# Kernel optimization log

Measured on AMD Instinct MI355X. Metric: run time of the kernel, lower is better.

The kernel has to match this reference:

```python
import jax, jax.numpy as jnp
import numpy as np

HIDDEN = 2048
HEADS = 16
HEAD_DIM = HIDDEN // HEADS


def setup_inputs() -> dict:
    key = jax.random.key(0)
    ks = jax.random.split(key, 5)
    scale = 1.0 / np.sqrt(HIDDEN)
    x = jax.random.normal(ks[0], (2, 2048, HIDDEN), dtype=jnp.float32)
    wq = jax.random.normal(ks[1], (HIDDEN, HIDDEN), dtype=jnp.float32) * scale
    wk = jax.random.normal(ks[2], (HIDDEN, HIDDEN), dtype=jnp.float32) * scale
    wv = jax.random.normal(ks[3], (HIDDEN, HIDDEN), dtype=jnp.float32) * scale
    wo = jax.random.normal(ks[4], (HIDDEN, HIDDEN), dtype=jnp.float32) * scale
    return {"x": x, "wq": wq, "wk": wk, "wv": wv, "wo": wo}


def reference(x, wq, wk, wv, wo):
    B, S, D = x.shape
    # nn.Linear(w, bias=False): y = x @ w.T
    q = (x @ wq.T).reshape(B, S, HEADS, HEAD_DIM)
    k = (x @ wk.T).reshape(B, S, HEADS, HEAD_DIM)
    v = (x @ wv.T).reshape(B, S, HEADS, HEAD_DIM)
    scores = jnp.einsum("bqhd,bkhd->bhqk", q, k) / jnp.sqrt(
        jnp.asarray(HEAD_DIM, dtype=x.dtype)
    )
    causal_mask = jnp.triu(jnp.ones((S, S), dtype=bool), k=1)
    scores = jnp.where(causal_mask, -jnp.inf, scores)
    attn = jax.nn.softmax(scores, axis=-1)
    out = jnp.einsum("bhqk,bkhd->bqhd", attn, v).reshape(B, S, D)
    return out @ wo.T
```

## Files before the change

kernel.cpp:

```cpp
#include <hip/hip_runtime.h>
#include <hip/hip_bf16.h>
#include <math.h>

typedef unsigned short u16;
typedef __attribute__((ext_vector_type(8))) short bf16x8;
typedef __attribute__((ext_vector_type(4))) float f32x4;

__device__ static inline u16 f2bf(float f) {
  unsigned u = __float_as_uint(f);
  u += 0x7fff + ((u >> 16) & 1);
  return (u16)(u >> 16);
}

__device__ static inline void gload_lds16(const void* g, void* l) {
  __builtin_amdgcn_global_load_lds(
      (const __attribute__((address_space(1))) unsigned int*)g,
      (__attribute__((address_space(3))) unsigned int*)l, 16, 0, 0);
}

__device__ static inline void store_out(u16* p, float v)   { *p = f2bf(v); }
__device__ static inline void store_out(float* p, float v) { *p = v; }

__global__ void cvt_f32_bf16(const float* __restrict__ src, u16* __restrict__ dst, int n) {
  int stride = gridDim.x * blockDim.x;
  for (int i = blockIdx.x * blockDim.x + threadIdx.x; i * 8 < n; i += stride) {
    const float4* s4 = (const float4*)(src + (size_t)i * 8);
    float4 a = s4[0], b = s4[1];
    u16 t[8] = { f2bf(a.x), f2bf(a.y), f2bf(a.z), f2bf(a.w),
                 f2bf(b.x), f2bf(b.y), f2bf(b.z), f2bf(b.w) };
    *(bf16x8*)(dst + (size_t)i * 8) = *(bf16x8*)t;
  }
}

__global__ __launch_bounds__(512, 2)
void gemm_bt_256(const u16* __restrict__ A, const u16* __restrict__ Bm,
                 u16* __restrict__ C, int M, int N, int K) {
  __shared__ u16 Abuf[2][256 * 64];
  __shared__ u16 Bbuf[2][256 * 64];
  const int tid = threadIdx.x, lane = tid & 63, w = tid >> 6;
  const int wm = w >> 2, wn = w & 3;
  const int g = lane >> 4, l16 = lane & 15;

  const int per = gridDim.x >> 3;
  const int swz = ((int)blockIdx.x & 7) * per + ((int)blockIdx.x >> 3);
  const int nx = N >> 8;
  const int bx = swz % nx, by = swz / nx;
  const int brow = by << 8, bcol = bx << 8;
  const int nt = K >> 6;

  auto stage_half = [&](int sel, int kt, int d) {
    const u16* src = (sel < 2) ? A : Bm;
    const int rbase = (sel < 2) ? brow : bcol;
    const int h = sel & 1;
    char* lds = (char*)((sel < 2) ? Abuf[d] : Bbuf[d]) + h * 16384;
#pragma unroll
    for (int i = 0; i < 2; ++i) {
      int idx = i * 512 + tid;
      int r = h * 128 + (idx >> 3);
      int c = ((idx & 7) * 16) ^ ((r & 7) << 4);
      gload_lds16((const char*)(src + (size_t)(rbase + r) * K + kt * 64) + c,
                  lds + idx * 16);
    }
  };

  f32x4 acc[8][4] = {};
  bf16x8 afr[4][2], bfr0[2][2], bfr1[2][2];

  auto lda = [&](int d, int mf0) {
#pragma unroll
    for (int mf = 0; mf < 4; ++mf) {
      int r = wm * 128 + (mf0 + mf) * 16 + l16;
      const char* base = (const char*)Abuf[d] + r * 128;
      int sw = (r & 7) << 4;
#pragma unroll
      for (int ks = 0; ks < 2; ++ks)
        afr[mf][ks] = *(const bf16x8*)(base + ((ks * 64 + g * 16) ^ sw));
    }
  };
  auto ldb = [&](int d, int nf0, bf16x8 bf[2][2]) {
#pragma unroll
    for (int nf = 0; nf < 2; ++nf) {
      int r = wn * 64 + (nf0 + nf) * 16 + l16;
      const char* base = (const char*)Bbuf[d] + r * 128;
      int sw = (r & 7) << 4;
#pragma unroll
      for (int ks = 0; ks < 2; ++ks)
        bf[nf][ks] = *(const bf16x8*)(base + ((ks * 64 + g * 16) ^ sw));
    }
  };

#define WAIT_LGKM() do { \
    asm volatile("s_waitcnt lgkmcnt(0)" ::: "memory"); \
    __builtin_amdgcn_sched_barrier(0); } while (0)
#define QUAD(MF0, NF0, BFR) do { \
    __builtin_amdgcn_s_setprio(1); \
    _Pragma("unroll") for (int mf = 0; mf < 4; ++mf) \
    _Pragma("unroll") for (int nf = 0; nf < 2; ++nf) \
    _Pragma("unroll") for (int ks = 0; ks < 2; ++ks) \
      acc[MF0 + mf][NF0 + nf] = __builtin_amdgcn_mfma_f32_16x16x32_bf16( \
          afr[mf][ks], BFR[nf][ks], acc[MF0 + mf][NF0 + nf], 0, 0, 0); \
    __builtin_amdgcn_s_setprio(0); } while (0)

  stage_half(0, 0, 0); stage_half(1, 0, 0);
  stage_half(2, 0, 0); stage_half(3, 0, 0);
  stage_half(2, 1, 1); stage_half(3, 1, 1);
  asm volatile("s_waitcnt vmcnt(4)" ::: "memory");
  __builtin_amdgcn_sched_barrier(0);
  __builtin_amdgcn_s_barrier();

  for (int t = 0; t < nt; ++t) {
    const int cur = t & 1;
    lda(cur, 0); ldb(cur, 0, bfr0);
    if (t + 1 < nt) stage_half(0, t + 1, cur ^ 1);
    __builtin_amdgcn_s_barrier();
    WAIT_LGKM();
    QUAD(0, 0, bfr0);
    __builtin_amdgcn_s_barrier();
    ldb(cur, 2, bfr1);
    if (t + 1 < nt) stage_half(1, t + 1, cur ^ 1);
    __builtin_amdgcn_s_barrier();
    WAIT_LGKM();
    QUAD(0, 2, bfr1);
    __builtin_amdgcn_s_barrier();
    lda(cur, 4);
    if (t + 2 < nt) stage_half(2, t + 2, cur);
    __builtin_amdgcn_s_barrier();
    WAIT_LGKM();
    QUAD(4, 2, bfr1);
    __builtin_amdgcn_s_barrier();
    if (t + 2 < nt) stage_half(3, t + 2, cur);
    QUAD(4, 0, bfr0);
    if (t + 1 < nt) {
      if (t + 2 < nt) asm volatile("s_waitcnt vmcnt(4)" ::: "memory");
      else            asm volatile("s_waitcnt vmcnt(0)" ::: "memory");
      __builtin_amdgcn_sched_barrier(0);
      __builtin_amdgcn_s_barrier();
    }
  }
#undef WAIT_LGKM
#undef QUAD

  const size_t cb = (size_t)(brow + wm * 128) * N + bcol + wn * 64;
#pragma unroll
  for (int mf = 0; mf < 8; ++mf)
#pragma unroll
    for (int nf = 0; nf < 4; ++nf) {
      int col = nf * 16 + l16;
#pragma unroll
      for (int rr = 0; rr < 4; ++rr) {
        int row = mf * 16 + g * 4 + rr;
        C[cb + (size_t)row * N + col] = f2bf(acc[mf][nf][rr]);
      }
    }
}

template <typename OutT>
__global__ __launch_bounds__(256, 2)
void gemm_bt(const u16* __restrict__ A, const u16* __restrict__ Bm,
             OutT* __restrict__ C, int M, int N, int K) {
  __shared__ u16 As[128 * 32];
  __shared__ u16 Bs[128 * 32];
  const int tid = threadIdx.x;
  const int lane = tid & 63;
  const int w = tid >> 6, wr = w >> 1, wc = w & 1;
  const int g = lane >> 4, l16 = lane & 15;
  const int row0 = blockIdx.y * 128, col0 = blockIdx.x * 128;
  f32x4 acc[4][4] = {};

  for (int k0 = 0; k0 < K; k0 += 32) {
    __syncthreads();
#pragma unroll
    for (int i = 0; i < 2; ++i) {
      int idx = i * 256 + tid;
      int r = idx >> 2, c = (idx & 3) * 8;
      gload_lds16(A  + (size_t)(row0 + r) * K + k0 + c, As + idx * 8);
      gload_lds16(Bm + (size_t)(col0 + r) * K + k0 + c, Bs + idx * 8);
    }
    __syncthreads();
    bf16x8 af[4], bfr[4];
#pragma unroll
    for (int m2 = 0; m2 < 4; ++m2)
      af[m2] = *(const bf16x8*)(As + (wr * 64 + m2 * 16 + l16) * 32 + g * 8);
#pragma unroll
    for (int n2 = 0; n2 < 4; ++n2)
      bfr[n2] = *(const bf16x8*)(Bs + (wc * 64 + n2 * 16 + l16) * 32 + g * 8);
#pragma unroll
    for (int m2 = 0; m2 < 4; ++m2)
#pragma unroll
      for (int n2 = 0; n2 < 4; ++n2)
        acc[m2][n2] = __builtin_amdgcn_mfma_f32_16x16x32_bf16(af[m2], bfr[n2], acc[m2][n2], 0, 0, 0);
  }

#pragma unroll
  for (int m2 = 0; m2 < 4; ++m2)
#pragma unroll
    for (int n2 = 0; n2 < 4; ++n2) {
      int col = col0 + wc * 64 + n2 * 16 + l16;
#pragma unroll
      for (int r = 0; r < 4; ++r) {
        int row = row0 + wr * 64 + m2 * 16 + g * 4 + r;
        store_out(C + (size_t)row * N + col, acc[m2][n2][r]);
      }
    }
}

__global__ __launch_bounds__(256)
void transpose_v(const u16* __restrict__ QKV, u16* __restrict__ Vt) {
  __shared__ u16 t[64][72];
  const int tid = threadIdx.x;
  const int b = blockIdx.y >> 5;
  const int s0 = (blockIdx.y & 31) * 64;
  const int hd0 = blockIdx.x * 64;
  const int lr = tid >> 2, lc = (tid & 3) * 16;
  const u16* src = QKV + ((size_t)(b * 2048 + s0 + lr) * 6144 + 4096 + hd0 + lc);
  *(bf16x8*)&t[lr][lc]     = *(const bf16x8*)src;
  *(bf16x8*)&t[lr][lc + 8] = *(const bf16x8*)(src + 8);
  __syncthreads();
  u16 tmp[16];
#pragma unroll
  for (int j = 0; j < 16; ++j) tmp[j] = t[lc + j][lr];
  u16* dst = Vt + ((size_t)(b * 2048 + hd0 + lr) * 2048 + s0 + lc);
  *(bf16x8*)dst       = *(bf16x8*)tmp;
  *(bf16x8*)(dst + 8) = *(bf16x8*)(tmp + 8);
}

__global__ __launch_bounds__(256, 2)
void attn_fwd(const u16* __restrict__ QKV, const u16* __restrict__ Vt,
              u16* __restrict__ AO) {
  __shared__ u16 Ks[64 * 128];
  __shared__ u16 Vs[128 * 64];
  __shared__ u16 Ps[4][16 * 64];
  const int tid = threadIdx.x, lane = tid & 63, w = tid >> 6;
  const int g = lane >> 4, l16 = lane & 15;
  const int bh = blockIdx.y, b = bh >> 4, h = bh & 15;
  const int fold = blockIdx.x;

  for (int phase = 0; phase < 2; ++phase) {
    const int qt = phase == 0 ? fold : 31 - fold;
    const int q0 = qt * 64 + w * 16;

    bf16x8 qf[4];
    {
      const u16* qrow = QKV + ((size_t)(b * 2048 + q0 + l16) * 6144 + h * 128 + g * 8);
#pragma unroll
      for (int c = 0; c < 4; ++c) qf[c] = *(const bf16x8*)(qrow + c * 32);
    }
    f32x4 o[8] = {};
    float mrun[4] = {-INFINITY, -INFINITY, -INFINITY, -INFINITY};
    float lrun[4] = {0.f, 0.f, 0.f, 0.f};

    const int kv_last = qt * 64;
    for (int kv0 = 0; kv0 <= kv_last; kv0 += 64) {
      __syncthreads();
#pragma unroll
      for (int i = 0; i < 4; ++i) {
        int idx = i * 256 + tid;
        {
          int row = idx >> 4;
          int scolb = ((idx & 15) * 16) ^ ((row & 7) << 4);
          gload_lds16((const char*)QKV +
                          ((size_t)(b * 2048 + kv0 + row) * 6144 + 2048 + h * 128) * 2 + scolb,
                      (char*)Ks + idx * 16);
        }
        {
          int d = idx >> 3;
          int vcolb = ((idx & 7) * 16) ^ ((d & 7) << 4);
          gload_lds16((const char*)Vt + ((size_t)(bh * 128 + d) * 2048 + kv0) * 2 + vcolb,
                      (char*)Vs + idx * 16);
        }
      }
      __syncthreads();

      f32x4 s[4];
#pragma unroll
      for (int kb = 0; kb < 4; ++kb) {
        f32x4 a = {};
        int row = kb * 16 + l16;
        int swzk = (row & 7) << 4;
#pragma unroll
        for (int c = 0; c < 4; ++c) {
          bf16x8 kf = *(const bf16x8*)((const char*)Ks + row * 256 + ((c * 64 + g * 16) ^ swzk));
          a = __builtin_amdgcn_mfma_f32_16x16x32_bf16(qf[c], kf, a, 0, 0, 0);
        }
        s[kb] = a * 0.08838834764831845f;
      }
      if (kv0 == kv_last) {
#pragma unroll
        for (int kb = 0; kb < 4; ++kb)
#pragma unroll
          for (int r = 0; r < 4; ++r)
            if (kv0 + kb * 16 + l16 > q0 + g * 4 + r) s[kb][r] = -INFINITY;
      }

      float mnew[4], al[4], rs[4];
#pragma unroll
      for (int r = 0; r < 4; ++r) {
        float t = fmaxf(fmaxf(s[0][r], s[1][r]), fmaxf(s[2][r], s[3][r]));
        t = fmaxf(t, __shfl_xor(t, 1));
        t = fmaxf(t, __shfl_xor(t, 2));
        t = fmaxf(t, __shfl_xor(t, 4));
        t = fmaxf(t, __shfl_xor(t, 8));
        mnew[r] = fmaxf(mrun[r], t);
        al[r] = __expf(mrun[r] - mnew[r]);
        mrun[r] = mnew[r];
        rs[r] = 0.f;
      }
      {
        int prow = g * 4;
#pragma unroll
        for (int kb = 0; kb < 4; ++kb)
#pragma unroll
          for (int r = 0; r < 4; ++r) {
            float p = __expf(s[kb][r] - mnew[r]);
            rs[r] += p;
            int row = prow + r;
            int byteoff = (kb * 32 + l16 * 2) ^ ((row & 7) << 4);
            *(u16*)((char*)Ps[w] + row * 128 + byteoff) = f2bf(p);
          }
      }
#pragma unroll
      for (int r = 0; r < 4; ++r) {
        float t = rs[r];
        t += __shfl_xor(t, 1);
        t += __shfl_xor(t, 2);
        t += __shfl_xor(t, 4);
        t += __shfl_xor(t, 8);
        lrun[r] = lrun[r] * al[r] + t;
      }
#pragma unroll
      for (int db = 0; db < 8; ++db)
#pragma unroll
        for (int r = 0; r < 4; ++r) o[db][r] *= al[r];

      bf16x8 pa[2];
      {
        int swzp = (l16 & 7) << 4;
#pragma unroll
        for (int ks = 0; ks < 2; ++ks)
          pa[ks] = *(const bf16x8*)((const char*)Ps[w] + l16 * 128 + ((ks * 64 + g * 16) ^ swzp));
      }
#pragma unroll
      for (int db = 0; db < 8; ++db) {
        int row = db * 16 + l16;
        int swzv = (row & 7) << 4;
#pragma unroll
        for (int ks = 0; ks < 2; ++ks) {
          bf16x8 vf = *(const bf16x8*)((const char*)Vs + row * 128 + ((ks * 64 + g * 16) ^ swzv));
          o[db] = __builtin_amdgcn_mfma_f32_16x16x32_bf16(pa[ks], vf, o[db], 0, 0, 0);
        }
      }
    }

#pragma unroll
    for (int r = 0; r < 4; ++r) {
      float rl = 1.0f / lrun[r];
      int q = q0 + g * 4 + r;
#pragma unroll
      for (int db = 0; db < 8; ++db)
        AO[(size_t)(b * 2048 + q) * 2048 + h * 128 + db * 16 + l16] = f2bf(o[db][r] * rl);
    }
  }
}

extern "C" void kernel_launch(void* const* d_in, const int* in_sizes, int n_in,
                              void* d_out, int out_size, void* d_ws, size_t ws_size,
                              hipStream_t stream) {
  const float* x  = (const float*)d_in[0];
  const float* wq = (const float*)d_in[1];
  const float* wk = (const float*)d_in[2];
  const float* wv = (const float*)d_in[3];
  const float* wo = (const float*)d_in[4];
  float* out = (float*)d_out;

  char* ws = (char*)d_ws;
  u16* Xb   = (u16*)(ws);
  u16* Wqkv = (u16*)(ws + ((size_t)16 << 20));
  u16* Wob  = (u16*)(ws + ((size_t)40 << 20));
  u16* QKV  = (u16*)(ws + ((size_t)48 << 20));
  u16* Vt   = (u16*)(ws + ((size_t)96 << 20));
  u16* AO   = (u16*)(ws + ((size_t)112 << 20));

  auto cvt = [&](const float* s, u16* d, int n) {
    int blocks = (n / 8 + 255) / 256;
    if (blocks > 2048) blocks = 2048;
    cvt_f32_bf16<<<blocks, 256, 0, stream>>>(s, d, n);
  };
  cvt(x,  Xb,              2 * 2048 * 2048);
  cvt(wq, Wqkv,            2048 * 2048);
  cvt(wk, Wqkv + 4194304,  2048 * 2048);
  cvt(wv, Wqkv + 8388608,  2048 * 2048);
  cvt(wo, Wob,             2048 * 2048);

  gemm_bt_256<<<384, 512, 0, stream>>>(Xb, Wqkv, QKV, 4096, 6144, 2048);
  transpose_v<<<dim3(32, 64), 256, 0, stream>>>(QKV, Vt);
  attn_fwd<<<dim3(16, 32), 256, 0, stream>>>(QKV, Vt, AO);
  gemm_bt<float><<<dim3(16, 32), 256, 0, stream>>>(AO, Wob, out, 4096, 2048, 2048);
}
```

Before: 413.6 us.

## Generalize 256-row GEMM to templated N-tile; use it for QKV and output projection

Replaces the 256x256 QKV GEMM with a templated two-phase kernel whose N tile is 64*NF. QKV now uses 256x192 tiles (512 blocks instead of 384) for better CU fill. The simple 128x128 output-projection GEMM is replaced by the same pipelined kernel with 256x128 tiles. The pipeline is restructured into two halves per k-step with fewer barriers, and B is staged as a single block per step. Smaller N tiles reduce operand reuse per block.

```diff
diff --git a/kernel.cpp b/kernel.cpp
--- a/kernel.cpp
+++ b/kernel.cpp
@@ -32,39 +32,49 @@
   }
 }
 
+template <int NF, typename OutT>
 __global__ __launch_bounds__(512, 2)
-void gemm_bt_256(const u16* __restrict__ A, const u16* __restrict__ Bm,
-                 u16* __restrict__ C, int M, int N, int K) {
+void gemm2ph(const u16* __restrict__ A, const u16* __restrict__ Bm,
+             OutT* __restrict__ C, int M, int N, int K) {
+  constexpr int BN = NF * 64;
   __shared__ u16 Abuf[2][256 * 64];
-  __shared__ u16 Bbuf[2][256 * 64];
+  __shared__ u16 Bbuf[2][BN * 64];
   const int tid = threadIdx.x, lane = tid & 63, w = tid >> 6;
   const int wm = w >> 2, wn = w & 3;
   const int g = lane >> 4, l16 = lane & 15;
 
   const int per = gridDim.x >> 3;
   const int swz = ((int)blockIdx.x & 7) * per + ((int)blockIdx.x >> 3);
-  const int nx = N >> 8;
+  const int nx = N / BN;
   const int bx = swz % nx, by = swz / nx;
-  const int brow = by << 8, bcol = bx << 8;
+  const int brow = by << 8, bcol = bx * BN;
   const int nt = K >> 6;
 
-  auto stage_half = [&](int sel, int kt, int d) {
-    const u16* src = (sel < 2) ? A : Bm;
-    const int rbase = (sel < 2) ? brow : bcol;
-    const int h = sel & 1;
-    char* lds = (char*)((sel < 2) ? Abuf[d] : Bbuf[d]) + h * 16384;
+  auto stage_Ah = [&](int h, int kt, int d) {
+    char* lds = (char*)Abuf[d] + h * 16384;
 #pragma unroll
     for (int i = 0; i < 2; ++i) {
       int idx = i * 512 + tid;
       int r = h * 128 + (idx >> 3);
       int c = ((idx & 7) * 16) ^ ((r & 7) << 4);
-      gload_lds16((const char*)(src + (size_t)(rbase + r) * K + kt * 64) + c,
+      gload_lds16((const char*)(A + (size_t)(brow + r) * K + kt * 64) + c,
                   lds + idx * 16);
     }
   };
-
-  f32x4 acc[8][4] = {};
-  bf16x8 afr[4][2], bfr0[2][2], bfr1[2][2];
+  auto stage_B = [&](int kt, int d) {
+    char* lds = (char*)Bbuf[d];
+#pragma unroll
+    for (int i = 0; i < NF; ++i) {
+      int idx = i * 512 + tid;
+      int r = idx >> 3;
+      int c = ((idx & 7) * 16) ^ ((r & 7) << 4);
+      gload_lds16((const char*)(Bm + (size_t)(bcol + r) * K + kt * 64) + c,
+                  lds + idx * 16);
+    }
+  };
+
+  f32x4 acc[8][NF] = {};
+  bf16x8 afr[4][2], bfr[NF][2];
 
   auto lda = [&](int d, int mf0) {
 #pragma unroll
@@ -77,129 +87,80 @@
         afr[mf][ks] = *(const bf16x8*)(base + ((ks * 64 + g * 16) ^ sw));
     }
   };
-  auto ldb = [&](int d, int nf0, bf16x8 bf[2][2]) {
-#pragma unroll
-    for (int nf = 0; nf < 2; ++nf) {
-      int r = wn * 64 + (nf0 + nf) * 16 + l16;
+  auto ldb = [&](int d) {
+#pragma unroll
+    for (int nf = 0; nf < NF; ++nf) {
+      int r = wn * (NF * 16) + nf * 16 + l16;
       const char* base = (const char*)Bbuf[d] + r * 128;
       int sw = (r & 7) << 4;
 #pragma unroll
       for (int ks = 0; ks < 2; ++ks)
-        bf[nf][ks] = *(const bf16x8*)(base + ((ks * 64 + g * 16) ^ sw));
-    }
+        bfr[nf][ks] = *(const bf16x8*)(base + ((ks * 64 + g * 16) ^ sw));
+    }
+  };
+  auto mma_half = [&](int mf0) {
+    __builtin_amdgcn_s_setprio(1);
+#pragma unroll
+    for (int mf = 0; mf < 4; ++mf)
+#pragma unroll
+      for (int nf = 0; nf < NF; ++nf)
+#pragma unroll
+        for (int ks = 0; ks < 2; ++ks)
+          acc[mf0 + mf][nf] = __builtin_amdgcn_mfma_f32_16x16x32_bf16(
+              afr[mf][ks], bfr[nf][ks], acc[mf0 + mf][nf], 0, 0, 0);
+    __builtin_amdgcn_s_setprio(0);
   };
 
 #define WAIT_LGKM() do { \
     asm volatile("s_waitcnt lgkmcnt(0)" ::: "memory"); \
     __builtin_amdgcn_sched_barrier(0); } while (0)
-#define QUAD(MF0, NF0, BFR) do { \
-    __builtin_amdgcn_s_setprio(1); \
-    _Pragma("unroll") for (int mf = 0; mf < 4; ++mf) \
-    _Pragma("unroll") for (int nf = 0; nf < 2; ++nf) \
-    _Pragma("unroll") for (int ks = 0; ks < 2; ++ks) \
-      acc[MF0 + mf][NF0 + nf] = __builtin_amdgcn_mfma_f32_16x16x32_bf16( \
-          afr[mf][ks], BFR[nf][ks], acc[MF0 + mf][NF0 + nf], 0, 0, 0); \
-    __builtin_amdgcn_s_setprio(0); } while (0)
-
-  stage_half(0, 0, 0); stage_half(1, 0, 0);
-  stage_half(2, 0, 0); stage_half(3, 0, 0);
-  stage_half(2, 1, 1); stage_half(3, 1, 1);
-  asm volatile("s_waitcnt vmcnt(4)" ::: "memory");
-  __builtin_amdgcn_sched_barrier(0);
+#define WAIT_VM_NF() do { \
+    if constexpr (NF == 3) asm volatile("s_waitcnt vmcnt(3)" ::: "memory"); \
+    else                   asm volatile("s_waitcnt vmcnt(2)" ::: "memory"); \
+    __builtin_amdgcn_sched_barrier(0); } while (0)
+
+  stage_Ah(0, 0, 0); stage_Ah(1, 0, 0);
+  stage_B(0, 0);
+  stage_B(1, 1);
+  WAIT_VM_NF();
   __builtin_amdgcn_s_barrier();
 
   for (int t = 0; t < nt; ++t) {
     const int cur = t & 1;
-    lda(cur, 0); ldb(cur, 0, bfr0);
-    if (t + 1 < nt) stage_half(0, t + 1, cur ^ 1);
+    lda(cur, 0); ldb(cur);
+    if (t + 1 < nt) stage_Ah(0, t + 1, cur ^ 1);
     __builtin_amdgcn_s_barrier();
     WAIT_LGKM();
-    QUAD(0, 0, bfr0);
+    mma_half(0);
     __builtin_amdgcn_s_barrier();
-    ldb(cur, 2, bfr1);
-    if (t + 1 < nt) stage_half(1, t + 1, cur ^ 1);
+    lda(cur, 4);
+    if (t + 1 < nt) stage_Ah(1, t + 1, cur ^ 1);
+    if (t + 2 < nt) stage_B(t + 2, cur);
     __builtin_amdgcn_s_barrier();
     WAIT_LGKM();
-    QUAD(0, 2, bfr1);
-    __builtin_amdgcn_s_barrier();
-    lda(cur, 4);
-    if (t + 2 < nt) stage_half(2, t + 2, cur);
-    __builtin_amdgcn_s_barrier();
-    WAIT_LGKM();
-    QUAD(4, 2, bfr1);
-    __builtin_amdgcn_s_barrier();
-    if (t + 2 < nt) stage_half(3, t + 2, cur);
-    QUAD(4, 0, bfr0);
+    mma_half(4);
     if (t + 1 < nt) {
-      if (t + 2 < nt) asm volatile("s_waitcnt vmcnt(4)" ::: "memory");
-      else            asm volatile("s_waitcnt vmcnt(0)" ::: "memory");
-      __builtin_amdgcn_sched_barrier(0);
+      if (t + 2 < nt) { WAIT_VM_NF(); }
+      else {
+        asm volatile("s_waitcnt vmcnt(0)" ::: "memory");
+        __builtin_amdgcn_sched_barrier(0);
+      }
       __builtin_amdgcn_s_barrier();
     }
   }
 #undef WAIT_LGKM
-#undef QUAD
-
-  const size_t cb = (size_t)(brow + wm * 128) * N + bcol + wn * 64;
+#undef WAIT_VM_NF
+
+  const size_t cb = (size_t)(brow + wm * 128) * N + bcol + wn * (NF * 16);
 #pragma unroll
   for (int mf = 0; mf < 8; ++mf)
 #pragma unroll
-    for (int nf = 0; nf < 4; ++nf) {
+    for (int nf = 0; nf < NF; ++nf) {
       int col = nf * 16 + l16;
 #pragma unroll
       for (int rr = 0; rr < 4; ++rr) {
         int row = mf * 16 + g * 4 + rr;
-        C[cb + (size_t)row * N + col] = f2bf(acc[mf][nf][rr]);
-      }
-    }
-}
-
-template <typename OutT>
-__global__ __launch_bounds__(256, 2)
-void gemm_bt(const u16* __restrict__ A, const u16* __restrict__ Bm,
-             OutT* __restrict__ C, int M, int N, int K) {
-  __shared__ u16 As[128 * 32];
-  __shared__ u16 Bs[128 * 32];
-  const int tid = threadIdx.x;
-  const int lane = tid & 63;
-  const int w = tid >> 6, wr = w >> 1, wc = w & 1;
-  const int g = lane >> 4, l16 = lane & 15;
-  const int row0 = blockIdx.y * 128, col0 = blockIdx.x * 128;
-  f32x4 acc[4][4] = {};
-
-  for (int k0 = 0; k0 < K; k0 += 32) {
-    __syncthreads();
-#pragma unroll
-    for (int i = 0; i < 2; ++i) {
-      int idx = i * 256 + tid;
-      int r = idx >> 2, c = (idx & 3) * 8;
-      gload_lds16(A  + (size_t)(row0 + r) * K + k0 + c, As + idx * 8);
-      gload_lds16(Bm + (size_t)(col0 + r) * K + k0 + c, Bs + idx * 8);
-    }
-    __syncthreads();
-    bf16x8 af[4], bfr[4];
-#pragma unroll
-    for (int m2 = 0; m2 < 4; ++m2)
-      af[m2] = *(const bf16x8*)(As + (wr * 64 + m2 * 16 + l16) * 32 + g * 8);
-#pragma unroll
-    for (int n2 = 0; n2 < 4; ++n2)
-      bfr[n2] = *(const bf16x8*)(Bs + (wc * 64 + n2 * 16 + l16) * 32 + g * 8);
-#pragma unroll
-    for (int m2 = 0; m2 < 4; ++m2)
-#pragma unroll
-      for (int n2 = 0; n2 < 4; ++n2)
-        acc[m2][n2] = __builtin_amdgcn_mfma_f32_16x16x32_bf16(af[m2], bfr[n2], acc[m2][n2], 0, 0, 0);
-  }
-
-#pragma unroll
-  for (int m2 = 0; m2 < 4; ++m2)
-#pragma unroll
-    for (int n2 = 0; n2 < 4; ++n2) {
-      int col = col0 + wc * 64 + n2 * 16 + l16;
-#pragma unroll
-      for (int r = 0; r < 4; ++r) {
-        int row = row0 + wr * 64 + m2 * 16 + g * 4 + r;
-        store_out(C + (size_t)row * N + col, acc[m2][n2][r]);
+        store_out(C + cb + (size_t)row * N + col, acc[mf][nf][rr]);
       }
     }
 }
@@ -391,8 +352,8 @@
   cvt(wv, Wqkv + 8388608,  2048 * 2048);
   cvt(wo, Wob,             2048 * 2048);
 
-  gemm_bt_256<<<384, 512, 0, stream>>>(Xb, Wqkv, QKV, 4096, 6144, 2048);
+  gemm2ph<3, u16><<<512, 512, 0, stream>>>(Xb, Wqkv, QKV, 4096, 6144, 2048);
   transpose_v<<<dim3(32, 64), 256, 0, stream>>>(QKV, Vt);
   attn_fwd<<<dim3(16, 32), 256, 0, stream>>>(QKV, Vt, AO);
-  gemm_bt<float><<<dim3(16, 32), 256, 0, stream>>>(AO, Wob, out, 4096, 2048, 2048);
-}
+  gemm2ph<2, float><<<256, 512, 0, stream>>>(AO, Wob, out, 4096, 2048, 2048);
+}
```

Measured after the change: 382.6 us. 1.08x faster.
